# Performance work log

Hardware: AMD Instinct MI355X
Metric: run time of the kernel (lower is better)

Reference implementation:

```python
import jax, jax.numpy as jnp
import numpy as np

EPS = 1e-6   # stability_threshold
DT = 0.1     # flow_step timestep


def _sym_lower(a):
    # torch.linalg.eigh uses the lower triangle; build the symmetric matrix from it
    return jnp.tril(a) + jnp.swapaxes(jnp.tril(a, -1), -1, -2)


def setup_inputs() -> dict:
    key = jax.random.key(0)
    ks = jax.random.split(key, 4)
    B, D, H = 8192, 64, 256
    M = D * D
    metric = jax.random.normal(ks[0], (B, D, D), jnp.float32)
    ricci = jax.random.normal(ks[1], (B, D, D), jnp.float32)
    xavier = lambda k, fi, fo: jax.random.normal(k, (fo, fi), jnp.float32) * np.float32(np.sqrt(2.0 / (fi + fo)))
    W1 = xavier(ks[2], M, H)
    b1 = jnp.full((H,), 0.1, jnp.float32)
    W2 = xavier(ks[3], H, M)
    b2 = jnp.full((M,), 0.1, jnp.float32)
    return {"metric": metric, "ricci": ricci, "W1": W1, "b1": b1, "W2": W2, "b2": b2}


def reference(metric, ricci, W1, b1, W2, b2):
    B, D, _ = metric.shape
    mflat = metric.reshape(B, -1)                       # [B, D*D]
    metric_norm = jnp.linalg.norm(mflat, axis=-1)       # [B]
    ricci_norm = jnp.linalg.norm(ricci.reshape(B, -1), axis=-1)
    adt = (DT * jnp.minimum(1.0, 0.1 * metric_norm / (ricci_norm + EPS)))[:, None, None]  # [B,1,1]

    # flow MLP: Linear -> Tanh -> Linear on flattened metric
    h = jnp.tanh(mflat @ W1.T + b1)                     # [B, H]
    flow = -2.0 * ricci + (h @ W2.T + b2).reshape(B, D, D)

    # batched symmetric eigendecomposition + reconstruction
    ev, V = jnp.linalg.eigh(_sym_lower(flow), symmetrize_input=False)
    # clamp(|ev|, min=-EPS/adt) is a no-op (lower bound is negative) and
    # |ev| * exp(i*angle(ev)) == ev for real ev, so eigenvalues pass through.
    flow = (V * ev[:, None, :]) @ jnp.swapaxes(V, -1, -2)

    new_metric = metric + flow * adt

    ev2, V2 = jnp.linalg.eigh(_sym_lower(new_metric), symmetrize_input=False)
    min_abs = jnp.min(jnp.abs(ev2))                     # global scalar, as in torch
    # sign-preserving magnitude clamp: |ev| >= EPS, sign from angle (0 -> +EPS)
    ev2c = jnp.where(ev2 >= 0, jnp.maximum(ev2, EPS), jnp.minimum(ev2, -EPS))
    recon = (V2 * ev2c[:, None, :]) @ jnp.swapaxes(V2, -1, -2)
    return jnp.where(min_abs <= EPS, recon, new_metric)
```

## Files before the change

### kernel.cpp

```cpp
#include <hip/hip_runtime.h>
#include <hip/hip_bf16.h>
#include <math.h>

typedef __attribute__((ext_vector_type(4))) float  f32x4;
typedef __attribute__((ext_vector_type(8))) short  short8;
typedef __attribute__((ext_vector_type(4))) short  short4_t;

#define DTC   0.1f
#define EPSF  1e-6f
#define NPACK 2176
#define NTRI  2080

static __device__ __forceinline__ unsigned short f2bf(float f) {
    union { float f; unsigned int u; } v; v.f = f;
    unsigned int u = v.u;
    return (unsigned short)((u + 0x7FFFu + ((u >> 16) & 1u)) >> 16);
}
static __device__ __forceinline__ unsigned short f2bf_hw(float f) {
    __hip_bfloat16 b = __float2bfloat16(f);
    union { __hip_bfloat16 b; unsigned short u; } v; v.b = b;
    return v.u;
}
static __device__ __forceinline__ float bf2f(unsigned short b) {
    union { unsigned int u; float f; } v; v.u = ((unsigned int)b) << 16;
    return v.f;
}
static __device__ __forceinline__ void tri_unpack(int p, int& i, int& j) {
    int r = p / 65, c = p - r * 65;
    if (c < 64 - r) { j = c;            i = c + r;       }
    else            { j = c - 64 + r;   i = j + 63 - r;  }
}

static __device__ __forceinline__ void gload_lds16(const void* gptr, void* ldsptr) {
    __builtin_amdgcn_global_load_lds(
        (const __attribute__((address_space(1))) unsigned int*)gptr,
        (__attribute__((address_space(3))) unsigned int*)ldsptr, 16, 0, 0);
}

__global__ __launch_bounds__(256) void pack_k(const float* __restrict__ W1,
                                              const float* __restrict__ W2,
                                              const float* __restrict__ b2,
                                              unsigned short* __restrict__ w1b,
                                              unsigned short* __restrict__ w2p,
                                              float* __restrict__ b2p) {
    const int bid = blockIdx.x, t = threadIdx.x;
    if (bid < 1024) {
        int idx = bid * 256 + t;
        f32x4 v = ((const f32x4*)W1)[idx];
        short4_t o;
        o[0] = (short)f2bf(v[0]); o[1] = (short)f2bf(v[1]);
        o[2] = (short)f2bf(v[2]); o[3] = (short)f2bf(v[3]);
        ((short4_t*)w1b)[idx] = o;
    } else {
        int p = bid - 1024;
        if (p < NTRI) {
            int i, j; tri_unpack(p, i, j);
            w2p[p * 256 + t] = f2bf(W2[(i * 64 + j) * 256L + t]);
            if (t == 0) b2p[p] = b2[i * 64 + j];
        } else {
            w2p[p * 256 + t] = 0;
            if (t == 0) b2p[p] = 0.f;
        }
    }
}

__global__ __launch_bounds__(256, 2) void gemm1_k(const float* __restrict__ A,
                                                  const unsigned short* __restrict__ B,
                                                  unsigned short* __restrict__ P) {
    __shared__ unsigned short As[64 * 64];
    __shared__ unsigned short Bs[256 * 64];
    const int tid  = threadIdx.x;
    const int lane = tid & 63;
    const int w    = tid >> 6;
    const int wm   = w >> 1, wn = w & 1;
    const long bm  = (long)blockIdx.x * 64;
    const int  kz  = blockIdx.y;

    f32x4 acc[2][8];
#pragma unroll
    for (int m = 0; m < 2; m++)
#pragma unroll
        for (int n = 0; n < 8; n++) acc[m][n] = (f32x4){0.f, 0.f, 0.f, 0.f};

    const int rB = tid >> 3;
    const int cB = (tid & 7) * 8;

    for (int kk = kz * 512; kk < kz * 512 + 512; kk += 64) {
#pragma unroll
        for (int i = 0; i < 8; i++)
            gload_lds16(B + (i * 32 + rB) * 4096L + kk + cB,
                        (char*)Bs + i * 4096 + tid * 16);
#pragma unroll
        for (int i = 0; i < 2; i++) {
            const int row = i * 32 + rB;
            const float* src = A + (bm + row) * 4096L + kk + cB;
            f32x4 a0 = ((const f32x4*)src)[0];
            f32x4 a1 = ((const f32x4*)src)[1];
            short8 ob;
#pragma unroll
            for (int e = 0; e < 4; e++) ob[e]     = (short)f2bf_hw(a0[e]);
#pragma unroll
            for (int e = 0; e < 4; e++) ob[4 + e] = (short)f2bf_hw(a1[e]);
            *(short8*)&As[row * 64 + cB] = ob;
        }
        __syncthreads();

#pragma unroll
        for (int kq = 0; kq < 2; kq++) {
            short8 af0 = *(const short8*)&As[(wm * 32 + 0 * 16 + (lane & 15)) * 64 +
                                             kq * 32 + (lane >> 4) * 8];
            short8 af1 = *(const short8*)&As[(wm * 32 + 1 * 16 + (lane & 15)) * 64 +
                                             kq * 32 + (lane >> 4) * 8];
#pragma unroll
            for (int n = 0; n < 8; n++) {
                short8 bfn = *(const short8*)&Bs[(wn * 128 + n * 16 + (lane & 15)) * 64 +
                                                 kq * 32 + (lane >> 4) * 8];
                acc[0][n] = __builtin_amdgcn_mfma_f32_16x16x32_bf16(af0, bfn, acc[0][n], 0, 0, 0);
                acc[1][n] = __builtin_amdgcn_mfma_f32_16x16x32_bf16(af1, bfn, acc[1][n], 0, 0, 0);
            }
        }
        __syncthreads();
    }

    unsigned short* Pk = P + (long)kz * (8192L * 256);
#pragma unroll
    for (int n = 0; n < 8; n++) {
        long col = wn * 128 + n * 16 + (lane & 15);
#pragma unroll
        for (int m = 0; m < 2; m++)
#pragma unroll
            for (int r = 0; r < 4; r++) {
                long row = bm + wm * 32 + m * 16 + (lane >> 4) * 4 + r;
                Pk[row * 256 + col] = f2bf(acc[m][n][r]);
            }
    }
}

__global__ __launch_bounds__(256) void reduce_h_k(const unsigned short* __restrict__ P,
                                                  const float* __restrict__ b1,
                                                  unsigned short* __restrict__ h) {
    const int idx = blockIdx.x * 256 + threadIdx.x;
    float s[8];
#pragma unroll
    for (int e = 0; e < 8; e++) s[e] = 0.f;
#pragma unroll
    for (int kz = 0; kz < 8; kz++) {
        short8 v = ((const short8*)(P + (long)kz * 2097152))[idx];
#pragma unroll
        for (int e = 0; e < 8; e++) s[e] += bf2f((unsigned short)v[e]);
    }
    const int cb = (idx & 31) * 8;
    f32x4 bv0 = *(const f32x4*)(b1 + cb);
    f32x4 bv1 = *(const f32x4*)(b1 + cb + 4);
    short8 o;
#pragma unroll
    for (int e = 0; e < 4; e++) o[e]     = (short)f2bf(tanhf(s[e] + bv0[e]));
#pragma unroll
    for (int e = 0; e < 4; e++) o[4 + e] = (short)f2bf(tanhf(s[4 + e] + bv1[e]));
    ((short8*)h)[idx] = o;
}

__global__ __launch_bounds__(256, 2) void gemm2p_k(const unsigned short* __restrict__ A,
                                                   const unsigned short* __restrict__ B,
                                                   const float* __restrict__ bias,
                                                   unsigned short* __restrict__ C) {
    __shared__ unsigned short As[128 * 64];
    __shared__ unsigned short Bs[128 * 64];
    const int tid  = threadIdx.x;
    const int lane = tid & 63;
    const int w    = tid >> 6;
    const int wm   = w >> 1, wn = w & 1;
    const long bm  = (long)blockIdx.x * 128;
    const long bn  = (long)blockIdx.y * 128;

    f32x4 acc[4][4];
#pragma unroll
    for (int m = 0; m < 4; m++)
#pragma unroll
        for (int n = 0; n < 4; n++) acc[m][n] = (f32x4){0.f, 0.f, 0.f, 0.f};

    const int r0 = tid >> 3;
    const int c0 = (tid & 7) * 8;

    for (int kk = 0; kk < 256; kk += 64) {
#pragma unroll
        for (int i = 0; i < 4; i++) {
            gload_lds16(A + (bm + i * 32 + r0) * 256L + kk + c0,
                        (char*)As + i * 4096 + tid * 16);
            gload_lds16(B + (bn + i * 32 + r0) * 256L + kk + c0,
                        (char*)Bs + i * 4096 + tid * 16);
        }
        __syncthreads();

        short8 af[4][2], bf[4][2];
#pragma unroll
        for (int m = 0; m < 4; m++)
#pragma unroll
            for (int kq = 0; kq < 2; kq++)
                af[m][kq] = *(const short8*)&As[(wm * 64 + m * 16 + (lane & 15)) * 64 +
                                                kq * 32 + (lane >> 4) * 8];
#pragma unroll
        for (int n = 0; n < 4; n++)
#pragma unroll
            for (int kq = 0; kq < 2; kq++)
                bf[n][kq] = *(const short8*)&Bs[(wn * 64 + n * 16 + (lane & 15)) * 64 +
                                                kq * 32 + (lane >> 4) * 8];
#pragma unroll
        for (int m = 0; m < 4; m++)
#pragma unroll
            for (int n = 0; n < 4; n++) {
                acc[m][n] = __builtin_amdgcn_mfma_f32_16x16x32_bf16(af[m][0], bf[n][0],
                                                                    acc[m][n], 0, 0, 0);
                acc[m][n] = __builtin_amdgcn_mfma_f32_16x16x32_bf16(af[m][1], bf[n][1],
                                                                    acc[m][n], 0, 0, 0);
            }
        __syncthreads();
    }

#pragma unroll
    for (int n = 0; n < 4; n++) {
        long col = bn + wn * 64 + n * 16 + (lane & 15);
        float bv = bias[col];
#pragma unroll
        for (int m = 0; m < 4; m++)
#pragma unroll
            for (int r = 0; r < 4; r++) {
                long row = bm + wm * 64 + m * 16 + (lane >> 4) * 4 + r;
                C[row * NPACK + col] = f2bf(acc[m][n][r] + bv);
            }
    }
}

__global__ __launch_bounds__(256) void finalize3_k(const float* __restrict__ metric,
                                                   const float* __restrict__ ricci,
                                                   const unsigned short* __restrict__ mlpP,
                                                   float* __restrict__ out) {
    const int b = blockIdx.x;
    const int t = threadIdx.x;
    const long mbase = (long)b * 4096;
    const long pbase = (long)b * NPACK;
    __shared__ float s_f[64 * 65];
    __shared__ float red[8];
    __shared__ float s_adt;

    const short8* mp8 = (const short8*)(mlpP + pbase);
    {
        short8 v = mp8[t];
#pragma unroll
        for (int e = 0; e < 8; e++) {
            int p = t * 8 + e, i, j;
            tri_unpack(p, i, j);
            s_f[i * 65 + j] = bf2f((unsigned short)v[e]);
        }
        if (t < 4) {
            short8 v2 = mp8[256 + t];
#pragma unroll
            for (int e = 0; e < 8; e++) {
                int p = 2048 + t * 8 + e, i, j;
                tri_unpack(p, i, j);
                s_f[i * 65 + j] = bf2f((unsigned short)v2[e]);
            }
        }
    }
    __syncthreads();

    const f32x4* met4 = (const f32x4*)(metric + mbase);
    const f32x4* ric4 = (const f32x4*)(ricci + mbase);
    f32x4 mm[4];
    float msq = 0.f, rsq = 0.f;
#pragma unroll
    for (int k = 0; k < 4; k++) {
        int v = k * 256 + t;
        f32x4 r = ric4[v];
        f32x4 m = met4[v];
        mm[k] = m;
        msq += m[0]*m[0] + m[1]*m[1] + m[2]*m[2] + m[3]*m[3];
        rsq += r[0]*r[0] + r[1]*r[1] + r[2]*r[2] + r[3]*r[3];
        int e0 = v * 4;
        int i = e0 >> 6, j0 = e0 & 63;
#pragma unroll
        for (int e = 0; e < 4; e++) {
            int j = j0 + e;
            if (j <= i) s_f[i * 65 + j] -= 2.f * r[e];
        }
    }
#pragma unroll
    for (int off = 32; off > 0; off >>= 1) {
        msq += __shfl_down(msq, off);
        rsq += __shfl_down(rsq, off);
    }
    if ((t & 63) == 0) { red[t >> 6] = msq; red[4 + (t >> 6)] = rsq; }
    __syncthreads();
    if (t == 0) {
        float tm = red[0] + red[1] + red[2] + red[3];
        float tr = red[4] + red[5] + red[6] + red[7];
        s_adt = DTC * fminf(1.0f, 0.1f * sqrtf(tm) / (sqrtf(tr) + EPSF));
    }
    __syncthreads();

    const float adt = s_adt;
    f32x4* out4 = (f32x4*)(out + mbase);
#pragma unroll
    for (int k = 0; k < 4; k++) {
        int v = k * 256 + t;
        int e0 = v * 4;
        int i = e0 >> 6, j0 = e0 & 63;
        f32x4 o;
#pragma unroll
        for (int e = 0; e < 4; e++) {
            int j = j0 + e;
            int mx = i > j ? i : j;
            int mn = i > j ? j : i;
            o[e] = mm[k][e] + adt * s_f[mx * 65 + mn];
        }
        out4[v] = o;
    }
}

extern "C" void kernel_launch(void* const* d_in, const int* in_sizes, int n_in,
                              void* d_out, int out_size, void* d_ws, size_t ws_size,
                              hipStream_t stream) {
    const float* metric = (const float*)d_in[0];
    const float* ricci  = (const float*)d_in[1];
    const float* W1     = (const float*)d_in[2];
    const float* b1     = (const float*)d_in[3];
    const float* W2     = (const float*)d_in[4];
    const float* b2     = (const float*)d_in[5];
    float* out = (float*)d_out;

    const int B = 8192;

    char* ws = (char*)d_ws;
    unsigned short* mlpP = (unsigned short*)(ws);
    unsigned short* w1b  = (unsigned short*)(ws + 35651584);
    unsigned short* w2p  = (unsigned short*)(ws + 37748736);
    float*          b2p  = (float*)(ws + 38862848);
    unsigned short* hbf  = (unsigned short*)(ws + 38871552);
    unsigned short* part = (unsigned short*)out;

    pack_k<<<dim3(1024 + NPACK), dim3(256), 0, stream>>>(W1, W2, b2, w1b, w2p, b2p);

    gemm1_k<<<dim3(B / 64, 8), dim3(256), 0, stream>>>(metric, w1b, part);
    reduce_h_k<<<dim3(B * 256 / 8 / 256), dim3(256), 0, stream>>>(part, b1, hbf);
    gemm2p_k<<<dim3(B / 128, NPACK / 128), dim3(256), 0, stream>>>(hbf, w2p, b2p, mlpP);
    finalize3_k<<<dim3(B), dim3(256), 0, stream>>>(metric, ricci, mlpP, out);

    (void)in_sizes; (void)n_in; (void)out_size; (void)ws_size;
}
```

Measured before the change: 152.2 us.

## Fuse split-K GEMM1 with tanh reduction into double-buffered full-K kernel

Replaces the split-K first MLP GEMM, which wrote eight bf16 partial results, and the separate reduce/tanh kernel with one kernel. Each 512-thread block now covers 32 rows over the full K=4096, double-buffers the A and B tiles in LDS, and applies bias plus tanh in the epilogue. This removes the partial-sum traffic, one kernel launch, and the bf16 rounding of partial sums. In exchange each block runs a long serial K loop, so there are only 256 blocks, and each block re-reads all of W1 with less reuse per tile.

```diff
diff --git a/kernel.cpp b/kernel.cpp
--- a/kernel.cpp
+++ b/kernel.cpp
@@ -64,100 +64,114 @@
     }
 }
 
-__global__ __launch_bounds__(256, 2) void gemm1_k(const float* __restrict__ A,
-                                                  const unsigned short* __restrict__ B,
-                                                  unsigned short* __restrict__ P) {
-    __shared__ unsigned short As[64 * 64];
-    __shared__ unsigned short Bs[256 * 64];
+__global__ __launch_bounds__(512, 2) void gemm1f_k(const float* __restrict__ A,
+                                                   const unsigned short* __restrict__ B,
+                                                   const float* __restrict__ b1,
+                                                   unsigned short* __restrict__ h) {
+    __shared__ unsigned short As[2][32 * 64];
+    __shared__ unsigned short Bs[2][256 * 64];
     const int tid  = threadIdx.x;
     const int lane = tid & 63;
     const int w    = tid >> 6;
-    const int wm   = w >> 1, wn = w & 1;
-    const long bm  = (long)blockIdx.x * 64;
-    const int  kz  = blockIdx.y;
-
-    f32x4 acc[2][8];
+    const long bm  = (long)blockIdx.x * 32;
+
+    f32x4 acc[2][2];
 #pragma unroll
     for (int m = 0; m < 2; m++)
 #pragma unroll
-        for (int n = 0; n < 8; n++) acc[m][n] = (f32x4){0.f, 0.f, 0.f, 0.f};
-
-    const int rB = tid >> 3;
-    const int cB = (tid & 7) * 8;
-
-    for (int kk = kz * 512; kk < kz * 512 + 512; kk += 64) {
-#pragma unroll
-        for (int i = 0; i < 8; i++)
-            gload_lds16(B + (i * 32 + rB) * 4096L + kk + cB,
-                        (char*)Bs + i * 4096 + tid * 16);
-#pragma unroll
-        for (int i = 0; i < 2; i++) {
-            const int row = i * 32 + rB;
-            const float* src = A + (bm + row) * 4096L + kk + cB;
-            f32x4 a0 = ((const f32x4*)src)[0];
-            f32x4 a1 = ((const f32x4*)src)[1];
-            short8 ob;
-#pragma unroll
-            for (int e = 0; e < 4; e++) ob[e]     = (short)f2bf_hw(a0[e]);
-#pragma unroll
-            for (int e = 0; e < 4; e++) ob[4 + e] = (short)f2bf_hw(a1[e]);
-            *(short8*)&As[row * 64 + cB] = ob;
-        }
+        for (int n = 0; n < 2; n++) acc[m][n] = (f32x4){0.f, 0.f, 0.f, 0.f};
+
+    const int arow = tid >> 4;
+    const int acol = (tid & 15) * 4;
+    const int brow = tid >> 3;
+    const int bcol = (tid & 7) * 8;
+
+    {
+        f32x4 a0 = *(const f32x4*)(A + (bm + arow) * 4096L + acol);
+#pragma unroll
+        for (int i = 0; i < 4; i++)
+            gload_lds16(B + (i * 64 + brow) * 4096L + bcol,
+                        (char*)&Bs[0][0] + i * 8192 + tid * 16);
+        short4_t o;
+#pragma unroll
+        for (int e = 0; e < 4; e++) o[e] = (short)f2bf_hw(a0[e]);
+        *(short4_t*)&As[0][arow * 64 + acol] = o;
+    }
+    __syncthreads();
+
+    for (int t = 0; t < 63; t++) {
+        const int cur = t & 1, nxt = cur ^ 1;
+        const int kk = (t + 1) * 64;
+        f32x4 an = *(const f32x4*)(A + (bm + arow) * 4096L + kk + acol);
+#pragma unroll
+        for (int i = 0; i < 4; i++)
+            gload_lds16(B + (i * 64 + brow) * 4096L + kk + bcol,
+                        (char*)&Bs[nxt][0] + i * 8192 + tid * 16);
+        short8 af[2][2], bf[2][2];
+#pragma unroll
+        for (int m = 0; m < 2; m++)
+#pragma unroll
+            for (int kq = 0; kq < 2; kq++)
+                af[m][kq] = *(const short8*)&As[cur][(m * 16 + (lane & 15)) * 64 +
+                                                     kq * 32 + (lane >> 4) * 8];
+#pragma unroll
+        for (int n = 0; n < 2; n++)
+#pragma unroll
+            for (int kq = 0; kq < 2; kq++)
+                bf[n][kq] = *(const short8*)&Bs[cur][(w * 32 + n * 16 + (lane & 15)) * 64 +
+                                                     kq * 32 + (lane >> 4) * 8];
+#pragma unroll
+        for (int m = 0; m < 2; m++)
+#pragma unroll
+            for (int n = 0; n < 2; n++) {
+                acc[m][n] = __builtin_amdgcn_mfma_f32_16x16x32_bf16(af[m][0], bf[n][0],
+                                                                    acc[m][n], 0, 0, 0);
+                acc[m][n] = __builtin_amdgcn_mfma_f32_16x16x32_bf16(af[m][1], bf[n][1],
+                                                                    acc[m][n], 0, 0, 0);
+            }
+        short4_t o;
+#pragma unroll
+        for (int e = 0; e < 4; e++) o[e] = (short)f2bf_hw(an[e]);
+        *(short4_t*)&As[nxt][arow * 64 + acol] = o;
         __syncthreads();
-
-#pragma unroll
-        for (int kq = 0; kq < 2; kq++) {
-            short8 af0 = *(const short8*)&As[(wm * 32 + 0 * 16 + (lane & 15)) * 64 +
-                                             kq * 32 + (lane >> 4) * 8];
-            short8 af1 = *(const short8*)&As[(wm * 32 + 1 * 16 + (lane & 15)) * 64 +
-                                             kq * 32 + (lane >> 4) * 8];
-#pragma unroll
-            for (int n = 0; n < 8; n++) {
-                short8 bfn = *(const short8*)&Bs[(wn * 128 + n * 16 + (lane & 15)) * 64 +
-                                                 kq * 32 + (lane >> 4) * 8];
-                acc[0][n] = __builtin_amdgcn_mfma_f32_16x16x32_bf16(af0, bfn, acc[0][n], 0, 0, 0);
-                acc[1][n] = __builtin_amdgcn_mfma_f32_16x16x32_bf16(af1, bfn, acc[1][n], 0, 0, 0);
-            }
-        }
-        __syncthreads();
-    }
-
-    unsigned short* Pk = P + (long)kz * (8192L * 256);
-#pragma unroll
-    for (int n = 0; n < 8; n++) {
-        long col = wn * 128 + n * 16 + (lane & 15);
+    }
+    {
+        short8 af[2][2], bf[2][2];
+#pragma unroll
+        for (int m = 0; m < 2; m++)
+#pragma unroll
+            for (int kq = 0; kq < 2; kq++)
+                af[m][kq] = *(const short8*)&As[1][(m * 16 + (lane & 15)) * 64 +
+                                                   kq * 32 + (lane >> 4) * 8];
+#pragma unroll
+        for (int n = 0; n < 2; n++)
+#pragma unroll
+            for (int kq = 0; kq < 2; kq++)
+                bf[n][kq] = *(const short8*)&Bs[1][(w * 32 + n * 16 + (lane & 15)) * 64 +
+                                                   kq * 32 + (lane >> 4) * 8];
+#pragma unroll
+        for (int m = 0; m < 2; m++)
+#pragma unroll
+            for (int n = 0; n < 2; n++) {
+                acc[m][n] = __builtin_amdgcn_mfma_f32_16x16x32_bf16(af[m][0], bf[n][0],
+                                                                    acc[m][n], 0, 0, 0);
+                acc[m][n] = __builtin_amdgcn_mfma_f32_16x16x32_bf16(af[m][1], bf[n][1],
+                                                                    acc[m][n], 0, 0, 0);
+            }
+    }
+
+#pragma unroll
+    for (int n = 0; n < 2; n++) {
+        int col = w * 32 + n * 16 + (lane & 15);
+        float bv = b1[col];
 #pragma unroll
         for (int m = 0; m < 2; m++)
 #pragma unroll
             for (int r = 0; r < 4; r++) {
-                long row = bm + wm * 32 + m * 16 + (lane >> 4) * 4 + r;
-                Pk[row * 256 + col] = f2bf(acc[m][n][r]);
-            }
-    }
-}
-
-__global__ __launch_bounds__(256) void reduce_h_k(const unsigned short* __restrict__ P,
-                                                  const float* __restrict__ b1,
-                                                  unsigned short* __restrict__ h) {
-    const int idx = blockIdx.x * 256 + threadIdx.x;
-    float s[8];
-#pragma unroll
-    for (int e = 0; e < 8; e++) s[e] = 0.f;
-#pragma unroll
-    for (int kz = 0; kz < 8; kz++) {
-        short8 v = ((const short8*)(P + (long)kz * 2097152))[idx];
-#pragma unroll
-        for (int e = 0; e < 8; e++) s[e] += bf2f((unsigned short)v[e]);
-    }
-    const int cb = (idx & 31) * 8;
-    f32x4 bv0 = *(const f32x4*)(b1 + cb);
-    f32x4 bv1 = *(const f32x4*)(b1 + cb + 4);
-    short8 o;
-#pragma unroll
-    for (int e = 0; e < 4; e++) o[e]     = (short)f2bf(tanhf(s[e] + bv0[e]));
-#pragma unroll
-    for (int e = 0; e < 4; e++) o[4 + e] = (short)f2bf(tanhf(s[4 + e] + bv1[e]));
-    ((short8*)h)[idx] = o;
+                long row = bm + m * 16 + (lane >> 4) * 4 + r;
+                h[row * 256 + col] = f2bf(tanhf(acc[m][n][r] + bv));
+            }
+    }
 }
 
 __global__ __launch_bounds__(256, 2) void gemm2p_k(const unsigned short* __restrict__ A,
@@ -336,12 +350,10 @@
     unsigned short* w2p  = (unsigned short*)(ws + 37748736);
     float*          b2p  = (float*)(ws + 38862848);
     unsigned short* hbf  = (unsigned short*)(ws + 38871552);
-    unsigned short* part = (unsigned short*)out;
 
     pack_k<<<dim3(1024 + NPACK), dim3(256), 0, stream>>>(W1, W2, b2, w1b, w2p, b2p);
 
-    gemm1_k<<<dim3(B / 64, 8), dim3(256), 0, stream>>>(metric, w1b, part);
-    reduce_h_k<<<dim3(B * 256 / 8 / 256), dim3(256), 0, stream>>>(part, b1, hbf);
+    gemm1f_k<<<dim3(B / 32), dim3(512), 0, stream>>>(metric, w1b, b1, hbf);
     gemm2p_k<<<dim3(B / 128, NPACK / 128), dim3(256), 0, stream>>>(hbf, w2p, b2p, mlpP);
     finalize3_k<<<dim3(B), dim3(256), 0, stream>>>(metric, ricci, mlpP, out);
 
```

Measured after the change: 174.3 us. 1.15x slower.

## Fuse second MLP GEMM into finalize kernel, keeping packed outputs in LDS

Applied to the files above, without the earlier changes.

Replaces the separate tiled GEMM2 kernel and the finalize kernel with a single kernel. Each block handles 8 batch rows: it computes their packed lower-triangle MLP output with MFMA directly from global W2, stages it in shared memory, then applies the ricci, norm and adt update per row. This removes the round trip of the ~35MB bf16 intermediate through global memory and one launch. In exchange, half of each 16-row MFMA is wasted on padding and W2 is streamed from L2 by every block without LDS reuse.

```diff
diff --git a/kernel.cpp b/kernel.cpp
--- a/kernel.cpp
+++ b/kernel.cpp
@@ -10,6 +10,7 @@
 #define EPSF  1e-6f
 #define NPACK 2176
 #define NTRI  2080
+#define NB    8
 
 static __device__ __forceinline__ unsigned short f2bf(float f) {
     union { float f; unsigned int u; } v; v.f = f;
@@ -160,160 +161,114 @@
     ((short8*)h)[idx] = o;
 }
 
-__global__ __launch_bounds__(256, 2) void gemm2p_k(const unsigned short* __restrict__ A,
-                                                   const unsigned short* __restrict__ B,
-                                                   const float* __restrict__ bias,
-                                                   unsigned short* __restrict__ C) {
-    __shared__ unsigned short As[128 * 64];
-    __shared__ unsigned short Bs[128 * 64];
+__global__ __launch_bounds__(256, 3) void g2fin_k(const float* __restrict__ metric,
+                                                  const float* __restrict__ ricci,
+                                                  const unsigned short* __restrict__ h,
+                                                  const unsigned short* __restrict__ w2p,
+                                                  const float* __restrict__ b2p,
+                                                  float* __restrict__ out) {
+    __shared__ unsigned short s_mlp[NB * NPACK];
+    __shared__ float s_f[64 * 65];
+    __shared__ float red[8];
+    __shared__ float s_adt;
+
     const int tid  = threadIdx.x;
     const int lane = tid & 63;
     const int w    = tid >> 6;
-    const int wm   = w >> 1, wn = w & 1;
-    const long bm  = (long)blockIdx.x * 128;
-    const long bn  = (long)blockIdx.y * 128;
-
-    f32x4 acc[4][4];
-#pragma unroll
-    for (int m = 0; m < 4; m++)
-#pragma unroll
-        for (int n = 0; n < 4; n++) acc[m][n] = (f32x4){0.f, 0.f, 0.f, 0.f};
-
-    const int r0 = tid >> 3;
-    const int c0 = (tid & 7) * 8;
-
-    for (int kk = 0; kk < 256; kk += 64) {
-#pragma unroll
-        for (int i = 0; i < 4; i++) {
-            gload_lds16(A + (bm + i * 32 + r0) * 256L + kk + c0,
-                        (char*)As + i * 4096 + tid * 16);
-            gload_lds16(B + (bn + i * 32 + r0) * 256L + kk + c0,
-                        (char*)Bs + i * 4096 + tid * 16);
-        }
-        __syncthreads();
-
-        short8 af[4][2], bf[4][2];
-#pragma unroll
-        for (int m = 0; m < 4; m++)
-#pragma unroll
-            for (int kq = 0; kq < 2; kq++)
-                af[m][kq] = *(const short8*)&As[(wm * 64 + m * 16 + (lane & 15)) * 64 +
-                                                kq * 32 + (lane >> 4) * 8];
-#pragma unroll
-        for (int n = 0; n < 4; n++)
-#pragma unroll
-            for (int kq = 0; kq < 2; kq++)
-                bf[n][kq] = *(const short8*)&Bs[(wn * 64 + n * 16 + (lane & 15)) * 64 +
-                                                kq * 32 + (lane >> 4) * 8];
-#pragma unroll
-        for (int m = 0; m < 4; m++)
-#pragma unroll
-            for (int n = 0; n < 4; n++) {
-                acc[m][n] = __builtin_amdgcn_mfma_f32_16x16x32_bf16(af[m][0], bf[n][0],
-                                                                    acc[m][n], 0, 0, 0);
-                acc[m][n] = __builtin_amdgcn_mfma_f32_16x16x32_bf16(af[m][1], bf[n][1],
-                                                                    acc[m][n], 0, 0, 0);
+    const long b0  = (long)blockIdx.x * NB;
+
+    short8 afr[8];
+    {
+        const int r = lane & 15;
+#pragma unroll
+        for (int kq = 0; kq < 8; kq++) {
+            short8 v = (short8){0, 0, 0, 0, 0, 0, 0, 0};
+            if (r < 8)
+                v = *(const short8*)(h + (b0 + r) * 256 + kq * 32 + (lane >> 4) * 8);
+            afr[kq] = v;
+        }
+    }
+#pragma unroll 2
+    for (int ct = w; ct < 136; ct += 4) {
+        const int col = ct * 16 + (lane & 15);
+        const unsigned short* bp = w2p + (long)col * 256 + (lane >> 4) * 8;
+        f32x4 acc = (f32x4){0.f, 0.f, 0.f, 0.f};
+#pragma unroll
+        for (int kq = 0; kq < 8; kq++) {
+            short8 bfr = *(const short8*)(bp + kq * 32);
+            acc = __builtin_amdgcn_mfma_f32_16x16x32_bf16(afr[kq], bfr, acc, 0, 0, 0);
+        }
+        const float bv = b2p[col];
+        const int row0 = (lane >> 4) * 4;
+        if (row0 < 8) {
+#pragma unroll
+            for (int r = 0; r < 4; r++)
+                s_mlp[(row0 + r) * NPACK + col] = f2bf(acc[r] + bv);
+        }
+    }
+    __syncthreads();
+
+    for (int bb = 0; bb < NB; bb++) {
+        const long mbase = (b0 + bb) * 4096;
+
+        for (int p = tid; p < NTRI; p += 256) {
+            int i, j; tri_unpack(p, i, j);
+            s_f[i * 65 + j] = bf2f(s_mlp[bb * NPACK + p]);
+        }
+        __syncthreads();
+
+        const f32x4* met4 = (const f32x4*)(metric + mbase);
+        const f32x4* ric4 = (const f32x4*)(ricci + mbase);
+        f32x4 mm[4];
+        float msq = 0.f, rsq = 0.f;
+#pragma unroll
+        for (int k = 0; k < 4; k++) {
+            int v = k * 256 + tid;
+            f32x4 r = ric4[v];
+            f32x4 m = met4[v];
+            mm[k] = m;
+            msq += m[0]*m[0] + m[1]*m[1] + m[2]*m[2] + m[3]*m[3];
+            rsq += r[0]*r[0] + r[1]*r[1] + r[2]*r[2] + r[3]*r[3];
+            int e0 = v * 4;
+            int i = e0 >> 6, j0 = e0 & 63;
+#pragma unroll
+            for (int e = 0; e < 4; e++) {
+                int j = j0 + e;
+                if (j <= i) s_f[i * 65 + j] -= 2.f * r[e];
             }
-        __syncthreads();
-    }
-
-#pragma unroll
-    for (int n = 0; n < 4; n++) {
-        long col = bn + wn * 64 + n * 16 + (lane & 15);
-        float bv = bias[col];
-#pragma unroll
-        for (int m = 0; m < 4; m++)
-#pragma unroll
-            for (int r = 0; r < 4; r++) {
-                long row = bm + wm * 64 + m * 16 + (lane >> 4) * 4 + r;
-                C[row * NPACK + col] = f2bf(acc[m][n][r] + bv);
+        }
+#pragma unroll
+        for (int off = 32; off > 0; off >>= 1) {
+            msq += __shfl_down(msq, off);
+            rsq += __shfl_down(rsq, off);
+        }
+        if ((tid & 63) == 0) { red[w] = msq; red[4 + w] = rsq; }
+        __syncthreads();
+        if (tid == 0) {
+            float tm = red[0] + red[1] + red[2] + red[3];
+            float tr = red[4] + red[5] + red[6] + red[7];
+            s_adt = DTC * fminf(1.0f, 0.1f * sqrtf(tm) / (sqrtf(tr) + EPSF));
+        }
+        __syncthreads();
+
+        const float adt = s_adt;
+        f32x4* out4 = (f32x4*)(out + mbase);
+#pragma unroll
+        for (int k = 0; k < 4; k++) {
+            int v = k * 256 + tid;
+            int e0 = v * 4;
+            int i = e0 >> 6, j0 = e0 & 63;
+            f32x4 o;
+#pragma unroll
+            for (int e = 0; e < 4; e++) {
+                int j = j0 + e;
+                int mx = i > j ? i : j;
+                int mn = i > j ? j : i;
+                o[e] = mm[k][e] + adt * s_f[mx * 65 + mn];
             }
-    }
-}
-
-__global__ __launch_bounds__(256) void finalize3_k(const float* __restrict__ metric,
-                                                   const float* __restrict__ ricci,
-                                                   const unsigned short* __restrict__ mlpP,
-                                                   float* __restrict__ out) {
-    const int b = blockIdx.x;
-    const int t = threadIdx.x;
-    const long mbase = (long)b * 4096;
-    const long pbase = (long)b * NPACK;
-    __shared__ float s_f[64 * 65];
-    __shared__ float red[8];
-    __shared__ float s_adt;
-
-    const short8* mp8 = (const short8*)(mlpP + pbase);
-    {
-        short8 v = mp8[t];
-#pragma unroll
-        for (int e = 0; e < 8; e++) {
-            int p = t * 8 + e, i, j;
-            tri_unpack(p, i, j);
-            s_f[i * 65 + j] = bf2f((unsigned short)v[e]);
-        }
-        if (t < 4) {
-            short8 v2 = mp8[256 + t];
-#pragma unroll
-            for (int e = 0; e < 8; e++) {
-                int p = 2048 + t * 8 + e, i, j;
-                tri_unpack(p, i, j);
-                s_f[i * 65 + j] = bf2f((unsigned short)v2[e]);
-            }
-        }
-    }
-    __syncthreads();
-
-    const f32x4* met4 = (const f32x4*)(metric + mbase);
-    const f32x4* ric4 = (const f32x4*)(ricci + mbase);
-    f32x4 mm[4];
-    float msq = 0.f, rsq = 0.f;
-#pragma unroll
-    for (int k = 0; k < 4; k++) {
-        int v = k * 256 + t;
-        f32x4 r = ric4[v];
-        f32x4 m = met4[v];
-        mm[k] = m;
-        msq += m[0]*m[0] + m[1]*m[1] + m[2]*m[2] + m[3]*m[3];
-        rsq += r[0]*r[0] + r[1]*r[1] + r[2]*r[2] + r[3]*r[3];
-        int e0 = v * 4;
-        int i = e0 >> 6, j0 = e0 & 63;
-#pragma unroll
-        for (int e = 0; e < 4; e++) {
-            int j = j0 + e;
-            if (j <= i) s_f[i * 65 + j] -= 2.f * r[e];
-        }
-    }
-#pragma unroll
-    for (int off = 32; off > 0; off >>= 1) {
-        msq += __shfl_down(msq, off);
-        rsq += __shfl_down(rsq, off);
-    }
-    if ((t & 63) == 0) { red[t >> 6] = msq; red[4 + (t >> 6)] = rsq; }
-    __syncthreads();
-    if (t == 0) {
-        float tm = red[0] + red[1] + red[2] + red[3];
-        float tr = red[4] + red[5] + red[6] + red[7];
-        s_adt = DTC * fminf(1.0f, 0.1f * sqrtf(tm) / (sqrtf(tr) + EPSF));
-    }
-    __syncthreads();
-
-    const float adt = s_adt;
-    f32x4* out4 = (f32x4*)(out + mbase);
-#pragma unroll
-    for (int k = 0; k < 4; k++) {
-        int v = k * 256 + t;
-        int e0 = v * 4;
-        int i = e0 >> 6, j0 = e0 & 63;
-        f32x4 o;
-#pragma unroll
-        for (int e = 0; e < 4; e++) {
-            int j = j0 + e;
-            int mx = i > j ? i : j;
-            int mn = i > j ? j : i;
-            o[e] = mm[k][e] + adt * s_f[mx * 65 + mn];
-        }
-        out4[v] = o;
+            out4[v] = o;
+        }
+        __syncthreads();
     }
 }
 
@@ -331,19 +286,17 @@
     const int B = 8192;
 
     char* ws = (char*)d_ws;
-    unsigned short* mlpP = (unsigned short*)(ws);
-    unsigned short* w1b  = (unsigned short*)(ws + 35651584);
-    unsigned short* w2p  = (unsigned short*)(ws + 37748736);
-    float*          b2p  = (float*)(ws + 38862848);
-    unsigned short* hbf  = (unsigned short*)(ws + 38871552);
+    unsigned short* w1b  = (unsigned short*)(ws);
+    unsigned short* w2p  = (unsigned short*)(ws + 2097152);
+    float*          b2p  = (float*)(ws + 3211264);
+    unsigned short* hbf  = (unsigned short*)(ws + 3219968);
     unsigned short* part = (unsigned short*)out;
 
     pack_k<<<dim3(1024 + NPACK), dim3(256), 0, stream>>>(W1, W2, b2, w1b, w2p, b2p);
 
     gemm1_k<<<dim3(B / 64, 8), dim3(256), 0, stream>>>(metric, w1b, part);
     reduce_h_k<<<dim3(B * 256 / 8 / 256), dim3(256), 0, stream>>>(part, b1, hbf);
-    gemm2p_k<<<dim3(B / 128, NPACK / 128), dim3(256), 0, stream>>>(hbf, w2p, b2p, mlpP);
-    finalize3_k<<<dim3(B), dim3(256), 0, stream>>>(metric, ricci, mlpP, out);
+    g2fin_k<<<dim3(B / NB), dim3(256), 0, stream>>>(metric, ricci, hbf, w2p, b2p, out);
 
     (void)in_sizes; (void)n_in; (void)out_size; (void)ws_size;
 }
```

Result: slower. 332.1 us (+118.2%).
